# Kernel tuning notes

Hardware: AMD Instinct MI355X
Metric: run time of the kernel (lower is better)

Reference implementation:

```python
import jax, jax.numpy as jnp
import numpy as np

D = 2048      # input_dim
E = 16        # num_experts
H = 1024      # expert_units
K = 4         # k_top
B = 4096      # batch


def setup_inputs() -> dict:
    key = jax.random.key(0)
    ks = jax.random.split(key, 7)
    s1 = 1.0 / np.sqrt(D)
    s2 = 1.0 / np.sqrt(H)
    return {
        "x": jax.random.normal(ks[0], (B, D), dtype=jnp.float32),
        "W1": jax.random.uniform(ks[1], (E, D, H), jnp.float32, -s1, s1),
        "b1": jax.random.uniform(ks[2], (E, H), jnp.float32, -s1, s1),
        "W2": jax.random.uniform(ks[3], (E, H, D), jnp.float32, -s2, s2),
        "b2": jax.random.uniform(ks[4], (E, D), jnp.float32, -s2, s2),
        "Wr": jax.random.uniform(ks[5], (D, E), jnp.float32, -s1, s1),
        "br": jax.random.uniform(ks[6], (E,), jnp.float32, -s1, s1),
    }


def reference(x, W1, b1, W2, b2, Wr, br):
    # Router + top-k (torch.topk returns sorted descending; lax.top_k matches)
    logits = x @ Wr + br                          # [B, E]
    top_w, top_i = jax.lax.top_k(logits, K)       # [B, K]
    top_w = jax.nn.softmax(top_w, axis=1)

    # Dense all-expert MLP (eval mode: dropout is identity)
    h = jax.nn.relu(jnp.einsum('bd,edh->beh', x, W1) + b1)   # [B, E, H]
    expert_out = jnp.einsum('beh,ehd->bed', h, W2) + b2      # [B, E, D]

    # mask/detach trick: forward value is unchanged (identity in fwd)
    mask = jax.nn.one_hot(top_i, E, dtype=expert_out.dtype).sum(axis=1)  # [B, E]
    m = mask[:, :, None]
    expert_out = expert_out * m + jax.lax.stop_gradient(expert_out * (1.0 - m))

    # Gather top-k experts and combine
    sel = jnp.take_along_axis(expert_out, top_i[:, :, None], axis=1)    # [B, K, D]
    out = (sel * top_w[:, :, None]).sum(axis=1)
    return out + x
```

## Files before the change

### kernel.cpp

```cpp
#include <hip/hip_runtime.h>
#include <math.h>

#define D_   2048
#define E_   16
#define H_   1024
#define KSEL 4
#define B_   4096
#define CAP  4096

typedef short bf16x8_t __attribute__((ext_vector_type(8)));
typedef float f32x4_t  __attribute__((ext_vector_type(4)));

__device__ __forceinline__ unsigned short f2bf(float f) {
  unsigned u = __float_as_uint(f);
  u += 0x7FFFu + ((u >> 16) & 1u);
  return (unsigned short)(u >> 16);
}

__device__ __forceinline__ float bf2f(unsigned short h) {
  unsigned u = (unsigned)h << 16;
  return __uint_as_float(u);
}

__device__ __forceinline__ void gld16(const void* g, void* l) {
  __builtin_amdgcn_global_load_lds(
      (const __attribute__((address_space(1))) unsigned int*)g,
      (__attribute__((address_space(3))) unsigned int*)l, 16, 0, 0);
}

__global__ void k_prep(const float* __restrict__ x, unsigned short* __restrict__ xb) {
  int i = blockIdx.x * 256 + threadIdx.x;
  float4 v = ((const float4*)x)[i];
  ushort4 o;
  o.x = f2bf(v.x); o.y = f2bf(v.y); o.z = f2bf(v.z); o.w = f2bf(v.w);
  ((ushort4*)xb)[i] = o;
}

__global__ void k_transw(const float* __restrict__ in, unsigned short* __restrict__ out,
                         int R, int C) {
  __shared__ float tile[32][33];
  size_t ebase = (size_t)blockIdx.z * R * C;
  in += ebase; out += ebase;
  int c0 = blockIdx.x * 32, r0 = blockIdx.y * 32;
  int tx = threadIdx.x;
#pragma unroll
  for (int i = threadIdx.y; i < 32; i += 8)
    tile[i][tx] = in[(size_t)(r0 + i) * C + c0 + tx];
  __syncthreads();
#pragma unroll
  for (int i = threadIdx.y; i < 32; i += 8)
    out[(size_t)(c0 + i) * R + r0 + tx] = f2bf(tile[tx][i]);
}

__global__ void k_transr(const float* __restrict__ in, float* __restrict__ out) {
  int i = blockIdx.x * 256 + threadIdx.x;
  int d = i >> 4, e = i & 15;
  out[e * D_ + d] = in[i];
}

__global__ __launch_bounds__(256) void k_router(
    const float* __restrict__ x, const float* __restrict__ wrT, const float* __restrict__ br,
    int* __restrict__ tops, float* __restrict__ topw) {
  int wid = threadIdx.x >> 6, lane = threadIdx.x & 63;
  int t = blockIdx.x * 4 + wid;
  float acc[E_];
#pragma unroll
  for (int e = 0; e < E_; e++) acc[e] = 0.f;
  const float4* xr = (const float4*)(x + (size_t)t * D_);
#pragma unroll
  for (int j = 0; j < D_ / 256; j++) {
    float4 xv = xr[j * 64 + lane];
#pragma unroll
    for (int e = 0; e < E_; e++) {
      float4 wv = ((const float4*)(wrT + (size_t)e * D_))[j * 64 + lane];
      acc[e] += xv.x * wv.x + xv.y * wv.y + xv.z * wv.z + xv.w * wv.w;
    }
  }
#pragma unroll
  for (int e = 0; e < E_; e++) {
    float v = acc[e];
    for (int m = 32; m >= 1; m >>= 1) v += __shfl_xor(v, m);
    acc[e] = v;
  }
  if (lane == 0) {
    float lg[E_];
#pragma unroll
    for (int e = 0; e < E_; e++) lg[e] = acc[e] + br[e];
    unsigned used = 0; int sel[KSEL]; float sv[KSEL];
    for (int k = 0; k < KSEL; k++) {
      float best = -1e30f; int bi = 0;
      for (int e = 0; e < E_; e++)
        if (!((used >> e) & 1u) && lg[e] > best) { best = lg[e]; bi = e; }
      used |= 1u << bi; sel[k] = bi; sv[k] = best;
    }
    float mx = sv[0], s = 0.f, w[KSEL];
    for (int k = 0; k < KSEL; k++) { w[k] = expf(sv[k] - mx); s += w[k]; }
    float inv = 1.f / s;
    int4 ti; float4 tw;
    ti.x = sel[0]; ti.y = sel[1]; ti.z = sel[2]; ti.w = sel[3];
    tw.x = w[0] * inv; tw.y = w[1] * inv; tw.z = w[2] * inv; tw.w = w[3] * inv;
    ((int4*)tops)[t] = ti;
    ((float4*)topw)[t] = tw;
  }
}

__global__ __launch_bounds__(256) void k_build(
    const int* __restrict__ tops, const float* __restrict__ topw,
    int* __restrict__ counts, int* __restrict__ ids, float* __restrict__ wts,
    int* __restrict__ inv) {
  int e = blockIdx.x;
  int tid = threadIdx.x, lane = tid & 63, wid = tid >> 6;
  __shared__ int wsum[4];
  __shared__ int red[4];
  int base = 0;
  int pre = 0;
  for (int c = 0; c < B_; c += 256) {
    int t = c + tid;
    int4 tk = ((const int4*)tops)[t];
    pre += (tk.x < e) + (tk.y < e) + (tk.z < e) + (tk.w < e);
    int k = -1;
    if (tk.x == e) k = 0; else if (tk.y == e) k = 1;
    else if (tk.z == e) k = 2; else if (tk.w == e) k = 3;
    unsigned long long mask = __ballot(k >= 0);
    int myoff = __popcll(mask & ((1ull << lane) - 1ull));
    if (lane == 0) wsum[wid] = __popcll(mask);
    __syncthreads();
    int woff = 0;
#pragma unroll
    for (int i = 0; i < 4; i++) if (i < wid) woff += wsum[i];
    int ctotal = wsum[0] + wsum[1] + wsum[2] + wsum[3];
    if (k >= 0) {
      int slot = base + woff + myoff;
      ids[e * CAP + slot] = t;
      wts[e * CAP + slot] = topw[t * 4 + k];
    }
    base += ctotal;
    __syncthreads();
  }
  if (tid == 0) counts[e] = base;
  for (int m = 32; m >= 1; m >>= 1) pre += __shfl_xor(pre, m);
  if (lane == 0) red[wid] = pre;
  __syncthreads();
  int offe = red[0] + red[1] + red[2] + red[3];
  for (int s = tid; s < base; s += 256) {
    int t = ids[e * CAP + s];
    int4 tk = ((const int4*)tops)[t];
    int k = (tk.x == e) ? 0 : (tk.y == e) ? 1 : (tk.z == e) ? 2 : 3;
    inv[t * 4 + k] = offe + s;
  }
}

__global__ __launch_bounds__(256) void k_gather(
    const float* __restrict__ x, const unsigned short* __restrict__ ybuf,
    const int* __restrict__ inv, float* __restrict__ out) {
  int t = blockIdx.x;
  int4 iv = ((const int4*)inv)[t];
  const ushort4* y0 = (const ushort4*)(ybuf + (size_t)iv.x * D_);
  const ushort4* y1 = (const ushort4*)(ybuf + (size_t)iv.y * D_);
  const ushort4* y2 = (const ushort4*)(ybuf + (size_t)iv.z * D_);
  const ushort4* y3 = (const ushort4*)(ybuf + (size_t)iv.w * D_);
  const float4* xr = (const float4*)(x + (size_t)t * D_);
  float4* orow = (float4*)(out + (size_t)t * D_);
#pragma unroll
  for (int i = threadIdx.x; i < D_ / 4; i += 256) {
    float4 v = xr[i];
    ushort4 a = y0[i], b = y1[i], c = y2[i], d = y3[i];
    v.x += bf2f(a.x) + bf2f(b.x) + bf2f(c.x) + bf2f(d.x);
    v.y += bf2f(a.y) + bf2f(b.y) + bf2f(c.y) + bf2f(d.y);
    v.z += bf2f(a.z) + bf2f(b.z) + bf2f(c.z) + bf2f(d.z);
    v.w += bf2f(a.w) + bf2f(b.w) + bf2f(c.w) + bf2f(d.w);
    orow[i] = v;
  }
}


__global__ __launch_bounds__(256, 2) void k_gemm1(
    const unsigned short* __restrict__ xb,
    const unsigned short* __restrict__ w1t,
    const float* __restrict__ b1,
    const int* __restrict__ ids, const int* __restrict__ counts,
    unsigned short* __restrict__ hbuf)
{
  __shared__ unsigned short As[128 * 64];
  __shared__ unsigned short Bs[256 * 64];
  int cnts[E_], offsv[E_], rowt[E_];
  int s = 0, ntr = 0;
#pragma unroll
  for (int e = 0; e < E_; e++) {
    cnts[e] = counts[e];
    offsv[e] = s; s += cnts[e];
    rowt[e] = (cnts[e] + 127) >> 7; ntr += rowt[e];
  }
  const int NS = H_ / 256;
  int totalTiles = ntr * NS;
  int tid = threadIdx.x, lane = tid & 63, wid = tid >> 6;
  int wr = wid >> 1, wc = wid & 1;
  int cr = lane >> 3, slot = lane & 7;
  int sw = (slot ^ cr) << 3;
  int hi = lane >> 4, cl = lane & 15;
  int bswz = (blockIdx.x & 7) * (gridDim.x >> 3) + (blockIdx.x >> 3);

  for (int tile = bswz; tile < totalTiles; tile += gridDim.x) {
    int slab = tile / ntr;
    int rtg = tile - slab * ntr;
    int n0 = slab << 8;
    int e = 0, base = 0;
    while (e < E_ - 1 && rtg >= base + rowt[e]) { base += rowt[e]; e++; }
    int rt = rtg - base;
    int cnt = cnts[e];
    int r0 = rt << 7;

    const unsigned short* a_src[4];
    const unsigned short* b_src[8];
    const unsigned short* wbase = w1t + (size_t)e * H_ * D_;
#pragma unroll
    for (int i = 0; i < 4; i++) {
      int chunk = wid * 4 + i;
      int rr = r0 + chunk * 8 + cr;
      int rc = min(rr, cnt - 1);
      int tok = ids[e * CAP + rc];
      a_src[i] = xb + (size_t)tok * D_ + sw;
    }
#pragma unroll
    for (int i = 0; i < 8; i++) {
      int chunk = wid * 8 + i;
      b_src[i] = wbase + (size_t)(n0 + chunk * 8 + cr) * D_ + sw;
    }
    f32x4_t acc[4][8];
#pragma unroll
    for (int m = 0; m < 4; m++)
#pragma unroll
      for (int n = 0; n < 8; n++) acc[m][n] = (f32x4_t){0.f, 0.f, 0.f, 0.f};

    for (int kt = 0; kt < D_; kt += 64) {
#pragma unroll
      for (int i = 0; i < 4; i++)
        gld16(a_src[i] + kt, As + (wid * 4 + i) * 512);
#pragma unroll
      for (int i = 0; i < 8; i++)
        gld16(b_src[i] + kt, Bs + (wid * 8 + i) * 512);
      __syncthreads();
#pragma unroll
      for (int kb = 0; kb < 2; kb++) {
        bf16x8_t af[4], bfr[8];
#pragma unroll
        for (int m = 0; m < 4; m++) {
          int row = wr * 64 + m * 16 + (lane & 15);
          int ss = (kb * 4 + (lane >> 4)) ^ (row & 7);
          af[m] = *(const bf16x8_t*)(As + row * 64 + ss * 8);
        }
#pragma unroll
        for (int n = 0; n < 8; n++) {
          int row = wc * 128 + n * 16 + (lane & 15);
          int ss = (kb * 4 + (lane >> 4)) ^ (row & 7);
          bfr[n] = *(const bf16x8_t*)(Bs + row * 64 + ss * 8);
        }
#pragma unroll
        for (int m = 0; m < 4; m++)
#pragma unroll
          for (int n = 0; n < 8; n++)
            acc[m][n] = __builtin_amdgcn_mfma_f32_16x16x32_bf16(af[m], bfr[n], acc[m][n], 0, 0, 0);
      }
      __syncthreads();
    }
    int offe = offsv[e];
    float bias[8];
#pragma unroll
    for (int n = 0; n < 8; n++)
      bias[n] = b1[e * H_ + n0 + wc * 128 + n * 16 + cl];
#pragma unroll
    for (int m = 0; m < 4; m++)
#pragma unroll
      for (int j = 0; j < 4; j++) {
        int sr = r0 + wr * 64 + m * 16 + hi * 4 + j;
        if (sr < cnt) {
          size_t rowb = (size_t)(offe + sr) * H_;
#pragma unroll
          for (int n = 0; n < 8; n++) {
            int col = n0 + wc * 128 + n * 16 + cl;
            float v = acc[m][n][j] + bias[n];
            v = v > 0.f ? v : 0.f;
            hbuf[rowb + col] = f2bf(v);
          }
        }
      }
  }
}

__global__ __launch_bounds__(256, 2) void k_gemm2(
    const unsigned short* __restrict__ hbuf,
    const unsigned short* __restrict__ w2t,
    const float* __restrict__ b2,
    const float* __restrict__ wts,
    const int* __restrict__ counts,
    unsigned short* __restrict__ ybuf)
{
  __shared__ unsigned short As[128 * 64];
  __shared__ unsigned short Bs[256 * 64];
  int cnts[E_], offsv[E_], rowt[E_];
  int s = 0, ntr = 0;
#pragma unroll
  for (int e = 0; e < E_; e++) {
    cnts[e] = counts[e];
    offsv[e] = s; s += cnts[e];
    rowt[e] = (cnts[e] + 127) >> 7; ntr += rowt[e];
  }
  const int NS = D_ / 256;
  int totalTiles = ntr * NS;
  int tid = threadIdx.x, lane = tid & 63, wid = tid >> 6;
  int wr = wid >> 1, wc = wid & 1;
  int cr = lane >> 3, slot = lane & 7;
  int sw = (slot ^ cr) << 3;
  int hi = lane >> 4, cl = lane & 15;
  int bswz = (blockIdx.x & 7) * (gridDim.x >> 3) + (blockIdx.x >> 3);

  for (int tile = bswz; tile < totalTiles; tile += gridDim.x) {
    int slab = tile / ntr;
    int rtg = tile - slab * ntr;
    int n0 = slab << 8;
    int e = 0, base = 0;
    while (e < E_ - 1 && rtg >= base + rowt[e]) { base += rowt[e]; e++; }
    int rt = rtg - base;
    int cnt = cnts[e];
    int r0 = rt << 7;
    int offe = offsv[e];

    const unsigned short* a_src[4];
    const unsigned short* b_src[8];
    const unsigned short* wbase = w2t + (size_t)e * D_ * H_;
#pragma unroll
    for (int i = 0; i < 4; i++) {
      int chunk = wid * 4 + i;
      int rr = r0 + chunk * 8 + cr;
      int rc = min(rr, cnt - 1);
      a_src[i] = hbuf + (size_t)(offe + rc) * H_ + sw;
    }
#pragma unroll
    for (int i = 0; i < 8; i++) {
      int chunk = wid * 8 + i;
      b_src[i] = wbase + (size_t)(n0 + chunk * 8 + cr) * H_ + sw;
    }
    f32x4_t acc[4][8];
#pragma unroll
    for (int m = 0; m < 4; m++)
#pragma unroll
      for (int n = 0; n < 8; n++) acc[m][n] = (f32x4_t){0.f, 0.f, 0.f, 0.f};

    for (int kt = 0; kt < H_; kt += 64) {
#pragma unroll
      for (int i = 0; i < 4; i++)
        gld16(a_src[i] + kt, As + (wid * 4 + i) * 512);
#pragma unroll
      for (int i = 0; i < 8; i++)
        gld16(b_src[i] + kt, Bs + (wid * 8 + i) * 512);
      __syncthreads();
#pragma unroll
      for (int kb = 0; kb < 2; kb++) {
        bf16x8_t af[4], bfr[8];
#pragma unroll
        for (int m = 0; m < 4; m++) {
          int row = wr * 64 + m * 16 + (lane & 15);
          int ss = (kb * 4 + (lane >> 4)) ^ (row & 7);
          af[m] = *(const bf16x8_t*)(As + row * 64 + ss * 8);
        }
#pragma unroll
        for (int n = 0; n < 8; n++) {
          int row = wc * 128 + n * 16 + (lane & 15);
          int ss = (kb * 4 + (lane >> 4)) ^ (row & 7);
          bfr[n] = *(const bf16x8_t*)(Bs + row * 64 + ss * 8);
        }
#pragma unroll
        for (int m = 0; m < 4; m++)
#pragma unroll
          for (int n = 0; n < 8; n++)
            acc[m][n] = __builtin_amdgcn_mfma_f32_16x16x32_bf16(af[m], bfr[n], acc[m][n], 0, 0, 0);
      }
      __syncthreads();
    }
    float bias[8];
#pragma unroll
    for (int n = 0; n < 8; n++)
      bias[n] = b2[e * D_ + n0 + wc * 128 + n * 16 + cl];
#pragma unroll
    for (int m = 0; m < 4; m++)
#pragma unroll
      for (int j = 0; j < 4; j++) {
        int sr = r0 + wr * 64 + m * 16 + hi * 4 + j;
        if (sr < cnt) {
          float w = wts[e * CAP + sr];
          unsigned short* yrow = ybuf + (size_t)(offe + sr) * D_;
#pragma unroll
          for (int n = 0; n < 8; n++) {
            int col = n0 + wc * 128 + n * 16 + cl;
            yrow[col] = f2bf(w * (acc[m][n][j] + bias[n]));
          }
        }
      }
  }
}

extern "C" void kernel_launch(void* const* d_in, const int* in_sizes, int n_in,
                              void* d_out, int out_size, void* d_ws, size_t ws_size,
                              hipStream_t stream) {
  const float* x  = (const float*)d_in[0];
  const float* W1 = (const float*)d_in[1];
  const float* b1 = (const float*)d_in[2];
  const float* W2 = (const float*)d_in[3];
  const float* b2 = (const float*)d_in[4];
  const float* Wr = (const float*)d_in[5];
  const float* br = (const float*)d_in[6];
  float* out = (float*)d_out;
  char* ws = (char*)d_ws;
  unsigned short* W1t  = (unsigned short*)(ws);
  unsigned short* ybuf = (unsigned short*)(ws);
  unsigned short* W2t  = (unsigned short*)(ws + 67108864);
  unsigned short* xb   = (unsigned short*)(ws + 134217728);
  unsigned short* hb   = (unsigned short*)(ws + 150994944);
  int*   ids    = (int*)  (ws + 184549376);
  float* wts    = (float*)(ws + 184811520);
  int*   counts = (int*)  (ws + 185073664);
  float* wrT    = (float*)(ws + 185073728);
  int*   tops   = (int*)  (ws + 185204800);
  float* topw   = (float*)(ws + 185270336);
  int*   inv    = (int*)  (ws + 185335872);

  k_prep<<<8192, 256, 0, stream>>>(x, xb);
  k_transr<<<128, 256, 0, stream>>>(Wr, wrT);
  k_transw<<<dim3(32, 64, 16), dim3(32, 8), 0, stream>>>(W1, W1t, 2048, 1024);
  k_transw<<<dim3(64, 32, 16), dim3(32, 8), 0, stream>>>(W2, W2t, 1024, 2048);
  k_router<<<1024, 256, 0, stream>>>(x, wrT, br, tops, topw);
  k_build<<<16, 256, 0, stream>>>(tops, topw, counts, ids, wts, inv);
  k_gemm1<<<512, 256, 0, stream>>>(xb, W1t, b1, ids, counts, hb);
  k_gemm2<<<1024, 256, 0, stream>>>(hb, W2t, b2, wts, counts, ybuf);
  k_gather<<<4096, 256, 0, stream>>>(x, ybuf, inv, out);
}
```

Before: 479.6 us.

## Shrink GEMM N-tile to 128, fuse bf16 cast into router, widen transpose stores

The x-to-bf16 conversion moves into the router kernel, which already reads x, so one launch and one full read of x go away. The weight-transpose kernel now uses a 1D block and writes packed ushort2 pairs, making its global stores wider. Both grouped GEMMs drop from 128x256 to 128x128 output tiles, with half the LDS, smaller accumulators, 3 blocks per CU and 768-block grids, trading per-tile operand reuse for occupancy and better load balance.

```diff
diff --git a/kernel.cpp b/kernel.cpp
--- a/kernel.cpp
+++ b/kernel.cpp
@@ -28,28 +28,25 @@
       (__attribute__((address_space(3))) unsigned int*)l, 16, 0, 0);
 }
 
-__global__ void k_prep(const float* __restrict__ x, unsigned short* __restrict__ xb) {
-  int i = blockIdx.x * 256 + threadIdx.x;
-  float4 v = ((const float4*)x)[i];
-  ushort4 o;
-  o.x = f2bf(v.x); o.y = f2bf(v.y); o.z = f2bf(v.z); o.w = f2bf(v.w);
-  ((ushort4*)xb)[i] = o;
-}
-
 __global__ void k_transw(const float* __restrict__ in, unsigned short* __restrict__ out,
                          int R, int C) {
   __shared__ float tile[32][33];
   size_t ebase = (size_t)blockIdx.z * R * C;
   in += ebase; out += ebase;
   int c0 = blockIdx.x * 32, r0 = blockIdx.y * 32;
-  int tx = threadIdx.x;
-#pragma unroll
-  for (int i = threadIdx.y; i < 32; i += 8)
+  int tx = threadIdx.x & 31, ty = threadIdx.x >> 5;
+#pragma unroll
+  for (int i = ty; i < 32; i += 8)
     tile[i][tx] = in[(size_t)(r0 + i) * C + c0 + tx];
   __syncthreads();
 #pragma unroll
-  for (int i = threadIdx.y; i < 32; i += 8)
-    out[(size_t)(c0 + i) * R + r0 + tx] = f2bf(tile[tx][i]);
+  for (int w = threadIdx.x; w < 32 * 16; w += 256) {
+    int i = w >> 4, rp = w & 15;
+    ushort2 v;
+    v.x = f2bf(tile[2 * rp][i]);
+    v.y = f2bf(tile[2 * rp + 1][i]);
+    *(ushort2*)(out + (size_t)(c0 + i) * R + r0 + 2 * rp) = v;
+  }
 }
 
 __global__ void k_transr(const float* __restrict__ in, float* __restrict__ out) {
@@ -60,16 +57,20 @@
 
 __global__ __launch_bounds__(256) void k_router(
     const float* __restrict__ x, const float* __restrict__ wrT, const float* __restrict__ br,
-    int* __restrict__ tops, float* __restrict__ topw) {
+    unsigned short* __restrict__ xb, int* __restrict__ tops, float* __restrict__ topw) {
   int wid = threadIdx.x >> 6, lane = threadIdx.x & 63;
   int t = blockIdx.x * 4 + wid;
   float acc[E_];
 #pragma unroll
   for (int e = 0; e < E_; e++) acc[e] = 0.f;
   const float4* xr = (const float4*)(x + (size_t)t * D_);
+  ushort4* xbw = (ushort4*)(xb + (size_t)t * D_);
 #pragma unroll
   for (int j = 0; j < D_ / 256; j++) {
     float4 xv = xr[j * 64 + lane];
+    ushort4 o;
+    o.x = f2bf(xv.x); o.y = f2bf(xv.y); o.z = f2bf(xv.z); o.w = f2bf(xv.w);
+    xbw[j * 64 + lane] = o;
 #pragma unroll
     for (int e = 0; e < E_; e++) {
       float4 wv = ((const float4*)(wrT + (size_t)e * D_))[j * 64 + lane];
@@ -174,7 +175,7 @@
 }
 
 
-__global__ __launch_bounds__(256, 2) void k_gemm1(
+__global__ __launch_bounds__(256, 3) void k_gemm1(
     const unsigned short* __restrict__ xb,
     const unsigned short* __restrict__ w1t,
     const float* __restrict__ b1,
@@ -182,7 +183,7 @@
     unsigned short* __restrict__ hbuf)
 {
   __shared__ unsigned short As[128 * 64];
-  __shared__ unsigned short Bs[256 * 64];
+  __shared__ unsigned short Bs[128 * 64];
   int cnts[E_], offsv[E_], rowt[E_];
   int s = 0, ntr = 0;
 #pragma unroll
@@ -191,7 +192,7 @@
     offsv[e] = s; s += cnts[e];
     rowt[e] = (cnts[e] + 127) >> 7; ntr += rowt[e];
   }
-  const int NS = H_ / 256;
+  const int NS = H_ / 128;
   int totalTiles = ntr * NS;
   int tid = threadIdx.x, lane = tid & 63, wid = tid >> 6;
   int wr = wid >> 1, wc = wid & 1;
@@ -203,7 +204,7 @@
   for (int tile = bswz; tile < totalTiles; tile += gridDim.x) {
     int slab = tile / ntr;
     int rtg = tile - slab * ntr;
-    int n0 = slab << 8;
+    int n0 = slab << 7;
     int e = 0, base = 0;
     while (e < E_ - 1 && rtg >= base + rowt[e]) { base += rowt[e]; e++; }
     int rt = rtg - base;
@@ -211,7 +212,7 @@
     int r0 = rt << 7;
 
     const unsigned short* a_src[4];
-    const unsigned short* b_src[8];
+    const unsigned short* b_src[4];
     const unsigned short* wbase = w1t + (size_t)e * H_ * D_;
 #pragma unroll
     for (int i = 0; i < 4; i++) {
@@ -220,29 +221,24 @@
       int rc = min(rr, cnt - 1);
       int tok = ids[e * CAP + rc];
       a_src[i] = xb + (size_t)tok * D_ + sw;
-    }
-#pragma unroll
-    for (int i = 0; i < 8; i++) {
-      int chunk = wid * 8 + i;
       b_src[i] = wbase + (size_t)(n0 + chunk * 8 + cr) * D_ + sw;
     }
-    f32x4_t acc[4][8];
+    f32x4_t acc[4][4];
 #pragma unroll
     for (int m = 0; m < 4; m++)
 #pragma unroll
-      for (int n = 0; n < 8; n++) acc[m][n] = (f32x4_t){0.f, 0.f, 0.f, 0.f};
+      for (int n = 0; n < 4; n++) acc[m][n] = (f32x4_t){0.f, 0.f, 0.f, 0.f};
 
     for (int kt = 0; kt < D_; kt += 64) {
 #pragma unroll
-      for (int i = 0; i < 4; i++)
+      for (int i = 0; i < 4; i++) {
         gld16(a_src[i] + kt, As + (wid * 4 + i) * 512);
-#pragma unroll
-      for (int i = 0; i < 8; i++)
-        gld16(b_src[i] + kt, Bs + (wid * 8 + i) * 512);
+        gld16(b_src[i] + kt, Bs + (wid * 4 + i) * 512);
+      }
       __syncthreads();
 #pragma unroll
       for (int kb = 0; kb < 2; kb++) {
-        bf16x8_t af[4], bfr[8];
+        bf16x8_t af[4], bfr[4];
 #pragma unroll
         for (int m = 0; m < 4; m++) {
           int row = wr * 64 + m * 16 + (lane & 15);
@@ -250,24 +246,24 @@
           af[m] = *(const bf16x8_t*)(As + row * 64 + ss * 8);
         }
 #pragma unroll
-        for (int n = 0; n < 8; n++) {
-          int row = wc * 128 + n * 16 + (lane & 15);
+        for (int n = 0; n < 4; n++) {
+          int row = wc * 64 + n * 16 + (lane & 15);
           int ss = (kb * 4 + (lane >> 4)) ^ (row & 7);
           bfr[n] = *(const bf16x8_t*)(Bs + row * 64 + ss * 8);
         }
 #pragma unroll
         for (int m = 0; m < 4; m++)
 #pragma unroll
-          for (int n = 0; n < 8; n++)
+          for (int n = 0; n < 4; n++)
             acc[m][n] = __builtin_amdgcn_mfma_f32_16x16x32_bf16(af[m], bfr[n], acc[m][n], 0, 0, 0);
       }
       __syncthreads();
     }
     int offe = offsv[e];
-    float bias[8];
-#pragma unroll
-    for (int n = 0; n < 8; n++)
-      bias[n] = b1[e * H_ + n0 + wc * 128 + n * 16 + cl];
+    float bias[4];
+#pragma unroll
+    for (int n = 0; n < 4; n++)
+      bias[n] = b1[e * H_ + n0 + wc * 64 + n * 16 + cl];
 #pragma unroll
     for (int m = 0; m < 4; m++)
 #pragma unroll
@@ -276,8 +272,8 @@
         if (sr < cnt) {
           size_t rowb = (size_t)(offe + sr) * H_;
 #pragma unroll
-          for (int n = 0; n < 8; n++) {
-            int col = n0 + wc * 128 + n * 16 + cl;
+          for (int n = 0; n < 4; n++) {
+            int col = n0 + wc * 64 + n * 16 + cl;
             float v = acc[m][n][j] + bias[n];
             v = v > 0.f ? v : 0.f;
             hbuf[rowb + col] = f2bf(v);
@@ -287,7 +283,7 @@
   }
 }
 
-__global__ __launch_bounds__(256, 2) void k_gemm2(
+__global__ __launch_bounds__(256, 3) void k_gemm2(
     const unsigned short* __restrict__ hbuf,
     const unsigned short* __restrict__ w2t,
     const float* __restrict__ b2,
@@ -296,7 +292,7 @@
     unsigned short* __restrict__ ybuf)
 {
   __shared__ unsigned short As[128 * 64];
-  __shared__ unsigned short Bs[256 * 64];
+  __shared__ unsigned short Bs[128 * 64];
   int cnts[E_], offsv[E_], rowt[E_];
   int s = 0, ntr = 0;
 #pragma unroll
@@ -305,7 +301,7 @@
     offsv[e] = s; s += cnts[e];
     rowt[e] = (cnts[e] + 127) >> 7; ntr += rowt[e];
   }
-  const int NS = D_ / 256;
+  const int NS = D_ / 128;
   int totalTiles = ntr * NS;
   int tid = threadIdx.x, lane = tid & 63, wid = tid >> 6;
   int wr = wid >> 1, wc = wid & 1;
@@ -317,7 +313,7 @@
   for (int tile = bswz; tile < totalTiles; tile += gridDim.x) {
     int slab = tile / ntr;
     int rtg = tile - slab * ntr;
-    int n0 = slab << 8;
+    int n0 = slab << 7;
     int e = 0, base = 0;
     while (e < E_ - 1 && rtg >= base + rowt[e]) { base += rowt[e]; e++; }
     int rt = rtg - base;
@@ -326,7 +322,7 @@
     int offe = offsv[e];
 
     const unsigned short* a_src[4];
-    const unsigned short* b_src[8];
+    const unsigned short* b_src[4];
     const unsigned short* wbase = w2t + (size_t)e * D_ * H_;
 #pragma unroll
     for (int i = 0; i < 4; i++) {
@@ -334,29 +330,24 @@
       int rr = r0 + chunk * 8 + cr;
       int rc = min(rr, cnt - 1);
       a_src[i] = hbuf + (size_t)(offe + rc) * H_ + sw;
-    }
-#pragma unroll
-    for (int i = 0; i < 8; i++) {
-      int chunk = wid * 8 + i;
       b_src[i] = wbase + (size_t)(n0 + chunk * 8 + cr) * H_ + sw;
     }
-    f32x4_t acc[4][8];
+    f32x4_t acc[4][4];
 #pragma unroll
     for (int m = 0; m < 4; m++)
 #pragma unroll
-      for (int n = 0; n < 8; n++) acc[m][n] = (f32x4_t){0.f, 0.f, 0.f, 0.f};
+      for (int n = 0; n < 4; n++) acc[m][n] = (f32x4_t){0.f, 0.f, 0.f, 0.f};
 
     for (int kt = 0; kt < H_; kt += 64) {
 #pragma unroll
-      for (int i = 0; i < 4; i++)
+      for (int i = 0; i < 4; i++) {
         gld16(a_src[i] + kt, As + (wid * 4 + i) * 512);
-#pragma unroll
-      for (int i = 0; i < 8; i++)
-        gld16(b_src[i] + kt, Bs + (wid * 8 + i) * 512);
+        gld16(b_src[i] + kt, Bs + (wid * 4 + i) * 512);
+      }
       __syncthreads();
 #pragma unroll
       for (int kb = 0; kb < 2; kb++) {
-        bf16x8_t af[4], bfr[8];
+        bf16x8_t af[4], bfr[4];
 #pragma unroll
         for (int m = 0; m < 4; m++) {
           int row = wr * 64 + m * 16 + (lane & 15);
@@ -364,23 +355,23 @@
           af[m] = *(const bf16x8_t*)(As + row * 64 + ss * 8);
         }
 #pragma unroll
-        for (int n = 0; n < 8; n++) {
-          int row = wc * 128 + n * 16 + (lane & 15);
+        for (int n = 0; n < 4; n++) {
+          int row = wc * 64 + n * 16 + (lane & 15);
           int ss = (kb * 4 + (lane >> 4)) ^ (row & 7);
           bfr[n] = *(const bf16x8_t*)(Bs + row * 64 + ss * 8);
         }
 #pragma unroll
         for (int m = 0; m < 4; m++)
 #pragma unroll
-          for (int n = 0; n < 8; n++)
+          for (int n = 0; n < 4; n++)
             acc[m][n] = __builtin_amdgcn_mfma_f32_16x16x32_bf16(af[m], bfr[n], acc[m][n], 0, 0, 0);
       }
       __syncthreads();
     }
-    float bias[8];
-#pragma unroll
-    for (int n = 0; n < 8; n++)
-      bias[n] = b2[e * D_ + n0 + wc * 128 + n * 16 + cl];
+    float bias[4];
+#pragma unroll
+    for (int n = 0; n < 4; n++)
+      bias[n] = b2[e * D_ + n0 + wc * 64 + n * 16 + cl];
 #pragma unroll
     for (int m = 0; m < 4; m++)
 #pragma unroll
@@ -390,8 +381,8 @@
           float w = wts[e * CAP + sr];
           unsigned short* yrow = ybuf + (size_t)(offe + sr) * D_;
 #pragma unroll
-          for (int n = 0; n < 8; n++) {
-            int col = n0 + wc * 128 + n * 16 + cl;
+          for (int n = 0; n < 4; n++) {
+            int col = n0 + wc * 64 + n * 16 + cl;
             yrow[col] = f2bf(w * (acc[m][n][j] + bias[n]));
           }
         }
@@ -424,13 +415,12 @@
   float* topw   = (float*)(ws + 185270336);
   int*   inv    = (int*)  (ws + 185335872);
 
-  k_prep<<<8192, 256, 0, stream>>>(x, xb);
   k_transr<<<128, 256, 0, stream>>>(Wr, wrT);
-  k_transw<<<dim3(32, 64, 16), dim3(32, 8), 0, stream>>>(W1, W1t, 2048, 1024);
-  k_transw<<<dim3(64, 32, 16), dim3(32, 8), 0, stream>>>(W2, W2t, 1024, 2048);
-  k_router<<<1024, 256, 0, stream>>>(x, wrT, br, tops, topw);
+  k_transw<<<dim3(32, 64, 16), 256, 0, stream>>>(W1, W1t, 2048, 1024);
+  k_transw<<<dim3(64, 32, 16), 256, 0, stream>>>(W2, W2t, 1024, 2048);
+  k_router<<<1024, 256, 0, stream>>>(x, wrT, br, xb, tops, topw);
   k_build<<<16, 256, 0, stream>>>(tops, topw, counts, ids, wts, inv);
-  k_gemm1<<<512, 256, 0, stream>>>(xb, W1t, b1, ids, counts, hb);
-  k_gemm2<<<1024, 256, 0, stream>>>(hb, W2t, b2, wts, counts, ybuf);
+  k_gemm1<<<768, 256, 0, stream>>>(xb, W1t, b1, ids, counts, hb);
+  k_gemm2<<<768, 256, 0, stream>>>(hb, W2t, b2, wts, counts, ybuf);
   k_gather<<<4096, 256, 0, stream>>>(x, ybuf, inv, out);
 }
```

New measurement: 442.2 us. -7.8%, faster.
